# Kernel optimization log

Hardware: AMD Instinct MI355X
Metric: run time of the kernel (lower is better)

## Reference

```python
import jax, jax.numpy as jnp
import numpy as np

B, T_ENC, T_DEC = 16, 256, 200
E, ATT, PRE, H, MEL, LOC, K = 512, 128, 256, 1024, 80, 32, 31


def setup_inputs() -> dict:
    key = jax.random.key(0)
    ks = jax.random.split(key, 20)
    s = lambda k, shape: jax.random.normal(k, shape, jnp.float32) * 0.02
    return dict(
        encoder_output=jax.random.normal(ks[0], (B, T_ENC, E), jnp.float32),
        padded_mels=jax.random.normal(ks[1], (B, T_DEC, MEL), jnp.float32),
        enc_proj_w=s(ks[2], (ATT, E)),
        lstm_proj_w=s(ks[3], (ATT, H)),
        loc_conv_w=s(ks[4], (LOC, 1, K)),
        loc_conv_b=jnp.zeros((LOC,), jnp.float32),
        loc_dense_w=s(ks[5], (ATT, LOC)),
        loc_dense_b=jnp.zeros((ATT,), jnp.float32),
        e_w=s(ks[6], (1, ATT)),
        e_b=jnp.zeros((1,), jnp.float32),
        prenet1_w=s(ks[7], (PRE, MEL)),
        prenet2_w=s(ks[8], (PRE, PRE)),
        w_ih0=s(ks[9], (4 * H, PRE + E)),
        w_hh0=s(ks[10], (4 * H, H)),
        b_ih0=jnp.zeros((4 * H,), jnp.float32),
        b_hh0=jnp.zeros((4 * H,), jnp.float32),
        w_ih1=s(ks[11], (4 * H, H)),
        w_hh1=s(ks[12], (4 * H, H)),
        b_ih1=jnp.zeros((4 * H,), jnp.float32),
        b_hh1=jnp.zeros((4 * H,), jnp.float32),
        proj_w=s(ks[13], (MEL, H + E)),
        proj_b=jnp.zeros((MEL,), jnp.float32),
        stop_w=s(ks[14], (1, H + E)),
        stop_b=jnp.zeros((1,), jnp.float32),
        text_lengths=jax.random.randint(ks[15], (B,), T_ENC // 2, T_ENC + 1),
    )


def _lstm_cell_zero(x, w_ih, b_ih, b_hh):
    # PyTorch LSTM cell with zero initial (h, c): h_prev contributes nothing
    # except the recurrent bias b_hh. Gate order: i, f, g, o.
    g = x @ w_ih.T + b_ih + b_hh
    i, f, gg, o = jnp.split(g, 4, axis=-1)
    c = jax.nn.sigmoid(i) * jnp.tanh(gg)  # f * c_prev == 0
    return jax.nn.sigmoid(o) * jnp.tanh(c)


def reference(encoder_output, padded_mels, enc_proj_w, lstm_proj_w, loc_conv_w,
              loc_conv_b, loc_dense_w, loc_dense_b, e_w, e_b, prenet1_w,
              prenet2_w, w_ih0, w_hh0, b_ih0, b_hh0, w_ih1, w_hh1, b_ih1,
              b_hh1, proj_w, proj_b, stop_w, stop_b, text_lengths):
    b, t_enc, _ = encoder_output.shape
    n_mel = padded_mels.shape[-1]
    h = w_hh0.shape[-1]
    pad = (loc_conv_w.shape[-1] - 1) // 2
    proc_enc = encoder_output @ enc_proj_w.T              # [B,Te,128]
    mask = jnp.arange(t_enc)[None, :] < text_lengths[:, None]
    # teacher forcing (ratio=1.0): prev mel at step t is padded_mels[:, t-1]
    prev_mels = jnp.concatenate(
        [jnp.zeros((b, 1, n_mel), padded_mels.dtype), padded_mels[:, :-1]],
        axis=1).transpose(1, 0, 2)                        # [Td,B,80]

    def step(carry, prev_mel):
        awc, h2 = carry                                   # [B,Te], [B,1024]
        # prenet (dropout omitted for a deterministic reference)
        x = jax.nn.relu(prev_mel @ prenet1_w.T)
        x = jax.nn.relu(x @ prenet2_w.T)                  # [B,256]
        # location-sensitive attention
        q = h2 @ lstm_proj_w.T                            # [B,128]
        loc = jax.lax.conv_general_dilated(
            awc[:, None, :], loc_conv_w, (1,), [(pad, pad)],
            dimension_numbers=('NCH', 'OIH', 'NCH')) + loc_conv_b[None, :, None]
        loc = jnp.einsum('bct,ac->bta', loc, loc_dense_w) + loc_dense_b
        en = jnp.tanh(q[:, None, :] + loc + proc_enc) @ e_w[0] + e_b[0]
        en = jnp.where(mask, en, -1e9)
        aw = jax.nn.softmax(en, axis=-1)                  # [B,Te]
        ctx = jnp.einsum('bt,bte->be', aw, encoder_output)  # [B,512]
        # 2-layer LSTM, state reset to zero every step (as in the original)
        li = jnp.concatenate([x, ctx], axis=-1)           # [B,768]
        h1 = _lstm_cell_zero(li, w_ih0, b_ih0, b_hh0)
        h2n = _lstm_cell_zero(h1, w_ih1, b_ih1, b_hh1)
        dec = jnp.concatenate([h2n, ctx], axis=-1)        # [B,1536]
        mel = dec @ proj_w.T + proj_b                     # [B,80]
        stop = (dec @ stop_w.T + stop_b)[:, 0]            # [B]
        return (awc + aw, h2n), (mel, stop)

    init = (jnp.zeros((b, t_enc), encoder_output.dtype),
            jnp.zeros((b, h), encoder_output.dtype))
    _, (mels, stops) = jax.lax.scan(step, init, prev_mels)
    return mels.transpose(1, 0, 2), stops.T               # [B,Td,80], [B,Td]
```

## Files before the change

kernel.cpp:

```cpp
#include <hip/hip_runtime.h>
#include <math.h>

#define NB   16
#define TE   256
#define TD   200
#define EE   512
#define ATT  128
#define PREN 256
#define HH   1024
#define NMEL 80
#define NLOC 32
#define KWW  31
#define PADW 15

#define OFF_X2   0
#define OFF_PE   (OFF_X2 + TD*NB*PREN)
#define OFF_AWC  (OFF_PE + NB*TE*ATT)
#define OFF_EN   (OFF_AWC + NB*TE)
#define OFF_Q    (OFF_EN + NB*TE)
#define OFF_CTX  (OFF_Q + NB*ATT)
#define OFF_H1   (OFF_CTX + NB*EE)
#define OFF_H2   (OFF_H1 + NB*HH)
#define OFF_BAR  (OFF_H2 + NB*HH)
#define BAR_U32  8192

#define ARR_G  0
#define ARR_L  4096

#define LW0_F4   (12*192)
#define LW1_F4   (12*256)
#define DYN_BYTES ((LW0_F4 + LW1_F4) * 16)

typedef float f4 __attribute__((ext_vector_type(4)));

__device__ __forceinline__ float sigmf(float x) { return 1.0f / (1.0f + expf(-x)); }
__device__ __forceinline__ float dot4(f4 a, f4 b) {
  return a.x*b.x + a.y*b.y + a.z*b.z + a.w*b.w;
}
__device__ __forceinline__ float red32(float v) {
  v += __shfl_down(v, 16, 32); v += __shfl_down(v, 8, 32);
  v += __shfl_down(v, 4, 32);  v += __shfl_down(v, 2, 32);
  v += __shfl_down(v, 1, 32);
  return v;
}

__device__ __forceinline__ unsigned ld_cg_u32(const unsigned* p) {
  unsigned r;
  asm volatile("global_load_dword %0, %1, off sc0 sc1\n\ts_waitcnt vmcnt(0)"
               : "=v"(r) : "v"(p) : "memory");
  return r;
}
__device__ __forceinline__ void st_cg_u32(unsigned* p, unsigned v) {
  asm volatile("global_store_dword %0, %1, off sc0 sc1" :: "v"(p), "v"(v) : "memory");
}
__device__ __forceinline__ float ld_cg_f32(const float* p) {
  float r;
  asm volatile("global_load_dword %0, %1, off sc0 sc1\n\ts_waitcnt vmcnt(0)"
               : "=v"(r) : "v"(p) : "memory");
  return r;
}
__device__ __forceinline__ void st_cg_f32(float* p, float v) {
  asm volatile("global_store_dword %0, %1, off sc0 sc1" :: "v"(p), "v"(v) : "memory");
}
__device__ __forceinline__ f4 ld_cg_f4(const f4* p) {
  f4 r;
  asm volatile("global_load_dwordx4 %0, %1, off sc0 sc1\n\ts_waitcnt vmcnt(0)"
               : "=v"(r) : "v"(p) : "memory");
  return r;
}
__device__ __forceinline__ void st_cg_f4(f4* p, f4 v) {
  asm volatile("global_store_dwordx4 %0, %1, off sc0 sc1" :: "v"(p), "v"(v) : "memory");
}
__device__ __forceinline__ void ld4_cg(f4& r0, f4& r1, f4& r2, f4& r3,
                                       const f4* a0, const f4* a1,
                                       const f4* a2, const f4* a3) {
  asm volatile(
    "global_load_dwordx4 %0, %4, off sc0 sc1\n\t"
    "global_load_dwordx4 %1, %5, off sc0 sc1\n\t"
    "global_load_dwordx4 %2, %6, off sc0 sc1\n\t"
    "global_load_dwordx4 %3, %7, off sc0 sc1\n\t"
    "s_waitcnt vmcnt(0)"
    : "=&v"(r0), "=&v"(r1), "=&v"(r2), "=&v"(r3)
    : "v"(a0), "v"(a1), "v"(a2), "v"(a3)
    : "memory");
}
__device__ __forceinline__ void ld8_cg(f4& r0, f4& r1, f4& r2, f4& r3,
                                       f4& r4, f4& r5, f4& r6, f4& r7,
                                       const f4* a0, const f4* a1, const f4* a2,
                                       const f4* a3, const f4* a4, const f4* a5,
                                       const f4* a6, const f4* a7) {
  asm volatile(
    "global_load_dwordx4 %0, %8, off sc0 sc1\n\t"
    "global_load_dwordx4 %1, %9, off sc0 sc1\n\t"
    "global_load_dwordx4 %2, %10, off sc0 sc1\n\t"
    "global_load_dwordx4 %3, %11, off sc0 sc1\n\t"
    "global_load_dwordx4 %4, %12, off sc0 sc1\n\t"
    "global_load_dwordx4 %5, %13, off sc0 sc1\n\t"
    "global_load_dwordx4 %6, %14, off sc0 sc1\n\t"
    "global_load_dwordx4 %7, %15, off sc0 sc1\n\t"
    "s_waitcnt vmcnt(0)"
    : "=&v"(r0), "=&v"(r1), "=&v"(r2), "=&v"(r3),
      "=&v"(r4), "=&v"(r5), "=&v"(r6), "=&v"(r7)
    : "v"(a0), "v"(a1), "v"(a2), "v"(a3),
      "v"(a4), "v"(a5), "v"(a6), "v"(a7)
    : "memory");
}

__device__ __forceinline__ void g_arrive(unsigned* bar, unsigned e) {
  __syncthreads();
  if (threadIdx.x == 0) st_cg_u32(bar + ARR_G + blockIdx.x * 16, e);
}
__device__ __forceinline__ void g_wait(unsigned* bar, unsigned e) {
  if (threadIdx.x < 256) {
    while (ld_cg_u32(bar + ARR_G + threadIdx.x * 16) < e) {}
  }
  __syncthreads();
}
__device__ __forceinline__ void l_arrive(unsigned* bar, unsigned e) {
  __syncthreads();
  if (threadIdx.x == 0) st_cg_u32(bar + ARR_L + blockIdx.x * 16, e);
}
__device__ __forceinline__ void l_wait(unsigned* bar, unsigned e, int b_grp) {
  if (threadIdx.x < 16) {
    while (ld_cg_u32(bar + ARR_L + (threadIdx.x * 16 + b_grp) * 16) < e) {}
  }
  __syncthreads();
}

__global__ void k_init(float* __restrict__ ws) {
  const int tid = threadIdx.x;
  float* awc = ws + OFF_AWC;
  float* qv  = ws + OFF_Q;
  unsigned* bar = (unsigned*)(ws + OFF_BAR);
  for (int i = tid; i < NB*TE; i += 256) st_cg_f32(awc + i, 0.0f);
  for (int i = tid; i < NB*ATT; i += 256) st_cg_f32(qv + i, 0.0f);
  for (int i = tid; i < BAR_U32; i += 256) st_cg_u32(bar + i, 0u);
}

__global__ void k_prenet(const float* __restrict__ mels,
                         const float* __restrict__ w1,
                         const float* __restrict__ w2,
                         float* __restrict__ x2) {
  const int t = blockIdx.x >> 4;
  const int b = blockIdx.x & 15;
  const int j = threadIdx.x;
  __shared__ float s_in[NMEL];
  __shared__ float s_x1[PREN];
  if (j < NMEL) s_in[j] = (t == 0) ? 0.0f : mels[(b*TD + (t-1))*NMEL + j];
  __syncthreads();
  float a1 = 0.0f;
  #pragma unroll 8
  for (int k = 0; k < NMEL; ++k) a1 += s_in[k] * w1[j*NMEL + k];
  s_x1[j] = fmaxf(a1, 0.0f);
  __syncthreads();
  float a2 = 0.0f;
  #pragma unroll 8
  for (int k = 0; k < PREN; ++k) a2 += s_x1[k] * w2[j*PREN + k];
  x2[(t*NB + b)*PREN + j] = fmaxf(a2, 0.0f);
}

__global__ void k_procenc(const float* __restrict__ enc,
                          const float* __restrict__ w,
                          float* __restrict__ pe) {
  const int bt = blockIdx.x;
  const int a = threadIdx.x;
  __shared__ float s_e[EE];
  for (int k = a; k < EE; k += 128) s_e[k] = enc[bt*EE + k];
  __syncthreads();
  float acc = 0.0f;
  #pragma unroll 8
  for (int k = 0; k < EE; ++k) acc += s_e[k] * w[a*EE + k];
  pe[bt*ATT + a] = acc;
}

__global__ void __launch_bounds__(512, 1) k_main(
    const float* __restrict__ enc,
    const float* __restrict__ lstm_proj_w,
    const float* __restrict__ loc_conv_w,
    const float* __restrict__ loc_conv_b,
    const float* __restrict__ loc_dense_w,
    const float* __restrict__ loc_dense_b,
    const float* __restrict__ e_w,
    const float* __restrict__ e_b,
    const float* __restrict__ w_ih0,
    const float* __restrict__ b_ih0,
    const float* __restrict__ b_hh0,
    const float* __restrict__ w_ih1,
    const float* __restrict__ b_ih1,
    const float* __restrict__ b_hh1,
    const float* __restrict__ proj_w,
    const float* __restrict__ proj_b,
    const float* __restrict__ stop_w,
    const float* __restrict__ stop_b,
    const int*   __restrict__ text_len,
    float* __restrict__ ws,
    float* __restrict__ out) {
  const int bid = blockIdx.x;
  const int tid = threadIdx.x;

  float* x2  = ws + OFF_X2;
  float* pe  = ws + OFF_PE;
  float* awc = ws + OFF_AWC;
  float* en  = ws + OFF_EN;
  float* qv  = ws + OFF_Q;
  float* ctx = ws + OFF_CTX;
  float* h1  = ws + OFF_H1;
  float* h2  = ws + OFF_H2;
  unsigned* bar = (unsigned*)(ws + OFF_BAR);

  __shared__ __align__(16) float s_ldw[NLOC*ATT];
  __shared__ float s_awc[64];
  __shared__ float s_loc[16*33];
  __shared__ float s_red[16];
  __shared__ float s_aw[256];
  __shared__ __align__(16) float s_dec[HH+EE];
  __shared__ float s_b0[12], s_b1[12];
  extern __shared__ __align__(16) float dynlds[];
  f4* lw0 = (f4*)dynlds;
  f4* lw1 = ((f4*)dynlds) + LW0_F4;

  const int b_grp = bid & 15;
  const int sub   = bid >> 4;
  const int h0    = bid * 4;

  for (int i = tid; i < NLOC*ATT; i += 512) {
    int c = i >> 7, a = i & 127;
    s_ldw[i] = loc_dense_w[a*NLOC + c];
  }
  if (tid < 12) {
    int g = tid >> 2, h = tid & 3;
    int gr = (g == 0 ? 0 : (g == 1 ? 2048 : 3072)) + h0 + h;
    s_b0[tid] = b_ih0[gr] + b_hh0[gr];
    s_b1[tid] = b_ih1[gr] + b_hh1[gr];
  }
  {
    const f4* w0_4 = (const f4*)w_ih0;
    const f4* w1_4 = (const f4*)w_ih1;
    for (int i = tid; i < LW0_F4; i += 512) {
      int r = i / 192, c = i - r*192;
      int g = r >> 2, h = r & 3;
      int grow = (g == 0 ? 0 : (g == 1 ? 2048 : 3072)) + h0 + h;
      lw0[i] = w0_4[grow*192 + c];
    }
    for (int i = tid; i < LW1_F4; i += 512) {
      int r = i >> 8, c = i & 255;
      int g = r >> 2, h = r & 3;
      int grow = (g == 0 ? 0 : (g == 1 ? 2048 : 3072)) + h0 + h;
      lw1[i] = w1_4[grow*256 + c];
    }
  }
  const int   lenb = text_len[b_grp];
  const float eb0  = e_b[0];

  const int tl = tid >> 5;
  const int j  = tid & 31;
  float lcw_r[KWW];
  #pragma unroll
  for (int k = 0; k < KWW; ++k) lcw_r[k] = loc_conv_w[j*KWW + k];
  const float lcb_r = loc_conv_b[j];
  const f4 db_r = *(const f4*)(loc_dense_b + 4*j);
  const f4 ew_r = *(const f4*)(e_w + 4*j);
  const f4 pe_r = *(const f4*)(pe + (size_t)(b_grp*TE + sub*16 + tl)*ATT + 4*j);
  const f4 ps_r = pe_r + db_r;
  const int e4i = tid >> 6;
  const int ts  = tid & 63;
  f4 encr[4];
  {
    const f4* enc4 = (const f4*)(enc + (size_t)b_grp*TE*EE);
    #pragma unroll
    for (int i = 0; i < 4; ++i)
      encr[i] = enc4[(size_t)(ts + 64*i)*(EE/4) + sub*8 + e4i];
  }
  const int pb = tid >> 5;
  const int kc = tid & 31;
  __syncthreads();

  unsigned eg = 0, el = 0;

  for (int t = 0; t < TD; ++t) {
    f4 pre;
    {
      if (tid >= 128 && tid < 176) {
        const int i = tid - 128;
        const int g = sub*16 - PADW + i;
        s_awc[i] = (i < 46 && g >= 0 && g < TE) ? ld_cg_f32(awc + b_grp*TE + g)
                                                : 0.0f;
      }
      __syncthreads();
      float cv = lcb_r;
      #pragma unroll
      for (int k = 0; k < KWW; ++k) cv += s_awc[tl + k] * lcw_r[k];
      s_loc[tl*33 + j] = cv;
      __syncthreads();
      f4 d4 = (f4){0.f, 0.f, 0.f, 0.f};
      #pragma unroll 8
      for (int c = 0; c < NLOC; ++c) {
        const float lv = s_loc[tl*33 + c];
        const f4 w4 = ((const f4*)s_ldw)[c*32 + j];
        d4.x += lv*w4.x; d4.y += lv*w4.y; d4.z += lv*w4.z; d4.w += lv*w4.w;
      }
      pre = ps_r + d4;
    }
    l_wait(bar, el, b_grp);
    {
      const f4 q4 = ld_cg_f4((const f4*)qv + b_grp*32 + j);
      float acc = tanhf(pre.x+q4.x)*ew_r.x + tanhf(pre.y+q4.y)*ew_r.y
                + tanhf(pre.z+q4.z)*ew_r.z + tanhf(pre.w+q4.w)*ew_r.w;
      acc = red32(acc);
      if (j == 0) {
        float evv = acc + eb0;
        const int tt = sub*16 + tl;
        if (tt >= lenb) evv = -1e9f;
        st_cg_f32(en + b_grp*TE + tt, evv);
      }
    }
    l_arrive(bar, ++el);
    l_wait(bar, el, b_grp);
    {
      float evv = 0.f, p = 0.f;
      if (tid < 256) {
        evv = ld_cg_f32(en + b_grp*TE + tid);
        float m = evv;
        #pragma unroll
        for (int d = 32; d > 0; d >>= 1) m = fmaxf(m, __shfl_xor(m, d));
        if ((tid & 63) == 0) s_red[tid >> 6] = m;
      }
      __syncthreads();
      const float mx = fmaxf(fmaxf(s_red[0], s_red[1]), fmaxf(s_red[2], s_red[3]));
      if (tid < 256) {
        p = expf(evv - mx);
        float sm = p;
        #pragma unroll
        for (int d = 32; d > 0; d >>= 1) sm += __shfl_xor(sm, d);
        if ((tid & 63) == 0) s_red[8 + (tid >> 6)] = sm;
      }
      __syncthreads();
      const float inv = 1.0f / (s_red[8] + s_red[9] + s_red[10] + s_red[11]);
      if (tid < 256) {
        const float aw = p * inv;
        s_aw[tid] = aw;
        if (sub == 0) {
          const float old = ld_cg_f32(awc + b_grp*TE + tid);
          st_cg_f32(awc + b_grp*TE + tid, old + aw);
        }
      }
      __syncthreads();
      f4 a4 = (f4){0.f, 0.f, 0.f, 0.f};
      #pragma unroll
      for (int i = 0; i < 4; ++i) {
        const float awv = s_aw[ts + 64*i];
        a4.x += awv*encr[i].x; a4.y += awv*encr[i].y;
        a4.z += awv*encr[i].z; a4.w += awv*encr[i].w;
      }
      #pragma unroll
      for (int d = 32; d > 0; d >>= 1) {
        a4.x += __shfl_down(a4.x, d);
        a4.y += __shfl_down(a4.y, d);
        a4.z += __shfl_down(a4.z, d);
        a4.w += __shfl_down(a4.w, d);
      }
      if (ts == 0) st_cg_f4((f4*)ctx + b_grp*(EE/4) + sub*8 + e4i, a4);
    }
    g_arrive(bar, ++eg);
    float acc[12];
    {
      #pragma unroll
      for (int r = 0; r < 12; ++r) acc[r] = 0.0f;
      const f4* x4p = (const f4*)(x2 + (size_t)(t*NB + pb)*PREN);
      #pragma unroll
      for (int i = 0; i < 2; ++i) {
        const int kf = kc + 32*i;
        const f4 xv = x4p[kf];
        #pragma unroll
        for (int r = 0; r < 12; ++r) acc[r] += dot4(xv, lw0[r*192 + kf]);
      }
    }
    g_wait(bar, eg);
    {
      const f4* c4p = (const f4*)(ctx + pb*EE);
      f4 cv0, cv1, cv2, cv3;
      ld4_cg(cv0, cv1, cv2, cv3, c4p+kc, c4p+kc+32, c4p+kc+64, c4p+kc+96);
      #pragma unroll
      for (int r = 0; r < 12; ++r) {
        acc[r] += dot4(cv0, lw0[r*192 + 64 + kc]);
        acc[r] += dot4(cv1, lw0[r*192 + 64 + kc + 32]);
        acc[r] += dot4(cv2, lw0[r*192 + 64 + kc + 64]);
        acc[r] += dot4(cv3, lw0[r*192 + 64 + kc + 96]);
      }
      #pragma unroll
      for (int r = 0; r < 12; ++r) acc[r] = red32(acc[r]);
      if (kc == 0) {
        f4 hv;
        #pragma unroll
        for (int h = 0; h < 4; ++h) {
          const float gi = acc[h]   + s_b0[h];
          const float gg = acc[4+h] + s_b0[4+h];
          const float go = acc[8+h] + s_b0[8+h];
          const float c = sigmf(gi) * tanhf(gg);
          hv[h] = sigmf(go) * tanhf(c);
        }
        st_cg_f4((f4*)h1 + pb*(HH/4) + bid, hv);
      }
    }
    g_arrive(bar, ++eg);
    g_wait(bar, eg);
    {
      #pragma unroll
      for (int r = 0; r < 12; ++r) acc[r] = 0.0f;
      const f4* h4p = (const f4*)(h1 + pb*HH);
      f4 hv0, hv1, hv2, hv3, hv4, hv5, hv6, hv7;
      ld8_cg(hv0, hv1, hv2, hv3, hv4, hv5, hv6, hv7,
             h4p+kc, h4p+kc+32, h4p+kc+64, h4p+kc+96,
             h4p+kc+128, h4p+kc+160, h4p+kc+192, h4p+kc+224);
      #pragma unroll
      for (int r = 0; r < 12; ++r) {
        acc[r] += dot4(hv0, lw1[r*256 + kc]);
        acc[r] += dot4(hv1, lw1[r*256 + kc + 32]);
        acc[r] += dot4(hv2, lw1[r*256 + kc + 64]);
        acc[r] += dot4(hv3, lw1[r*256 + kc + 96]);
        acc[r] += dot4(hv4, lw1[r*256 + kc + 128]);
        acc[r] += dot4(hv5, lw1[r*256 + kc + 160]);
        acc[r] += dot4(hv6, lw1[r*256 + kc + 192]);
        acc[r] += dot4(hv7, lw1[r*256 + kc + 224]);
      }
      #pragma unroll
      for (int r = 0; r < 12; ++r) acc[r] = red32(acc[r]);
      if (kc == 0) {
        f4 hv;
        #pragma unroll
        for (int h = 0; h < 4; ++h) {
          const float gi = acc[h]   + s_b1[h];
          const float gg = acc[4+h] + s_b1[4+h];
          const float go = acc[8+h] + s_b1[8+h];
          const float c = sigmf(gi) * tanhf(gg);
          hv[h] = sigmf(go) * tanhf(c);
        }
        st_cg_f4((f4*)h2 + pb*(HH/4) + bid, hv);
      }
    }
    g_arrive(bar, ++eg);
    if (tid >= 256 && tid < 384)
      ((f4*)s_dec)[tid] = ld_cg_f4((const f4*)ctx + b_grp*(EE/4) + (tid - 256));
    g_wait(bar, eg);
    {
      if (tid < 256)
        ((f4*)s_dec)[tid] = ld_cg_f4((const f4*)h2 + b_grp*(HH/4) + tid);
      __syncthreads();
      const int ol = tid >> 5;
      const int kq = tid & 31;
      const f4* s4 = (const f4*)s_dec;
      if (sub < 8) {
        const int a = sub*16 + ol;
        const f4* w4 = (const f4*)(lstm_proj_w + (size_t)a*HH);
        float a2 = 0.0f;
        #pragma unroll
        for (int i = 0; i < 8; ++i) a2 += dot4(s4[kq + 32*i], w4[kq + 32*i]);
        a2 = red32(a2);
        if (kq == 0) st_cg_f32(qv + b_grp*ATT + a, a2);
      } else {
        const int m = (sub - 8)*11 + ol;
        if (ol < 11 && m < 81) {
          const float* wrow = (m < NMEL) ? (proj_w + (size_t)m*(HH+EE)) : stop_w;
          const f4* w4 = (const f4*)wrow;
          float a2 = 0.0f;
          #pragma unroll
          for (int i = 0; i < 12; ++i) a2 += dot4(s4[kq + 32*i], w4[kq + 32*i]);
          a2 = red32(a2);
          if (kq == 0) {
            if (m < NMEL) out[(b_grp*TD + t)*NMEL + m] = a2 + proj_b[m];
            else          out[NB*TD*NMEL + b_grp*TD + t] = a2 + stop_b[0];
          }
        }
      }
    }
    l_arrive(bar, ++el);
  }
}

extern "C" void kernel_launch(void* const* d_in, const int* in_sizes, int n_in,
                              void* d_out, int out_size, void* d_ws, size_t ws_size,
                              hipStream_t stream) {
  (void)in_sizes; (void)n_in; (void)out_size; (void)ws_size;
  const float* enc         = (const float*)d_in[0];
  const float* mels        = (const float*)d_in[1];
  const float* enc_proj_w  = (const float*)d_in[2];
  const float* lstm_proj_w = (const float*)d_in[3];
  const float* loc_conv_w  = (const float*)d_in[4];
  const float* loc_conv_b  = (const float*)d_in[5];
  const float* loc_dense_w = (const float*)d_in[6];
  const float* loc_dense_b = (const float*)d_in[7];
  const float* e_w         = (const float*)d_in[8];
  const float* e_b         = (const float*)d_in[9];
  const float* prenet1_w   = (const float*)d_in[10];
  const float* prenet2_w   = (const float*)d_in[11];
  const float* w_ih0       = (const float*)d_in[12];
  const float* b_ih0       = (const float*)d_in[14];
  const float* b_hh0       = (const float*)d_in[15];
  const float* w_ih1       = (const float*)d_in[16];
  const float* b_ih1       = (const float*)d_in[18];
  const float* b_hh1       = (const float*)d_in[19];
  const float* proj_w      = (const float*)d_in[20];
  const float* proj_b      = (const float*)d_in[21];
  const float* stop_w      = (const float*)d_in[22];
  const float* stop_b      = (const float*)d_in[23];
  const int*   text_len    = (const int*)d_in[24];
  float* ws  = (float*)d_ws;
  float* out = (float*)d_out;

  static int attr_set = 0;
  if (!attr_set) {
    hipFuncSetAttribute((const void*)k_main,
                        hipFuncAttributeMaxDynamicSharedMemorySize, DYN_BYTES);
    attr_set = 1;
  }

  k_init<<<dim3(1), dim3(256), 0, stream>>>(ws);
  k_prenet<<<dim3(TD*NB), dim3(256), 0, stream>>>(mels, prenet1_w, prenet2_w, ws + OFF_X2);
  k_procenc<<<dim3(NB*TE), dim3(128), 0, stream>>>(enc, enc_proj_w, ws + OFF_PE);

  k_main<<<dim3(256), dim3(512), DYN_BYTES, stream>>>(
      enc, lstm_proj_w, loc_conv_w, loc_conv_b, loc_dense_w, loc_dense_b,
      e_w, e_b, w_ih0, b_ih0, b_hh0, w_ih1, b_ih1, b_hh1,
      proj_w, proj_b, stop_w, stop_b, text_len, ws, out);
}
```

Baseline: 4.471 ms.

## Use fp16 packed activations, flag-tagged records, and defer output projection

Stores the LDS-resident LSTM weights and the exchanged activations (prenet output, context, h1, h2, query) as packed fp16 and computes the dot products with fdot2. The global barriers around h2 and q are replaced by per-record step tags that consumers poll. The attention cumulative sum now lives in each block's shared memory instead of global memory. The mel/stop projection is moved to the next step's idle window, and the query projection is split across all 16 sub-blocks. The goal is fewer grid-wide barriers and less traffic per step, at the cost of fp16 rounding error and more intricate synchronisation.

```diff
diff --git a/kernel.cpp b/kernel.cpp
--- a/kernel.cpp
+++ b/kernel.cpp
@@ -13,25 +13,27 @@
 #define KWW  31
 #define PADW 15
 
-#define OFF_X2   0
-#define OFF_PE   (OFF_X2 + TD*NB*PREN)
-#define OFF_AWC  (OFF_PE + NB*TE*ATT)
-#define OFF_EN   (OFF_AWC + NB*TE)
-#define OFF_Q    (OFF_EN + NB*TE)
-#define OFF_CTX  (OFF_Q + NB*ATT)
-#define OFF_H1   (OFF_CTX + NB*EE)
-#define OFF_H2   (OFF_H1 + NB*HH)
-#define OFF_BAR  (OFF_H2 + NB*HH)
+#define OFF_X2H  0
+#define OFF_PE   (OFF_X2H + TD*NB*128)
+#define OFF_EN   (OFF_PE + NB*TE*ATT)
+#define OFF_CTH  (OFF_EN + NB*TE)
+#define OFF_H1H  (OFF_CTH + NB*256)
+#define OFF_H2R  (OFF_H1H + NB*512)
+#define OFF_QVR  (OFF_H2R + NB*256*4)
+#define OFF_BAR  (OFF_QVR + NB*16*2*4)
 #define BAR_U32  8192
-
-#define ARR_G  0
-#define ARR_L  4096
-
-#define LW0_F4   (12*192)
-#define LW1_F4   (12*256)
-#define DYN_BYTES ((LW0_F4 + LW1_F4) * 16)
+#define ARR_G 0
+#define ARR_L 4096
+
+#define LW0X_U32 (12*128)
+#define LW0C_U32 (12*256)
+#define LW1_U32  (12*512)
+#define DYN_BYTES ((LW0X_U32 + LW0C_U32 + LW1_U32)*4)
 
 typedef float f4 __attribute__((ext_vector_type(4)));
+typedef unsigned int u32x4 __attribute__((ext_vector_type(4)));
+typedef unsigned int u32x2 __attribute__((ext_vector_type(2)));
+typedef _Float16 h2t __attribute__((ext_vector_type(2)));
 
 __device__ __forceinline__ float sigmf(float x) { return 1.0f / (1.0f + expf(-x)); }
 __device__ __forceinline__ float dot4(f4 a, f4 b) {
@@ -43,6 +45,25 @@
   v += __shfl_down(v, 1, 32);
   return v;
 }
+__device__ __forceinline__ float red64(float v) {
+  v += __shfl_down(v, 32); v += __shfl_down(v, 16); v += __shfl_down(v, 8);
+  v += __shfl_down(v, 4);  v += __shfl_down(v, 2);  v += __shfl_down(v, 1);
+  return v;
+}
+__device__ __forceinline__ float fdot2(unsigned a, unsigned b, float c) {
+  return __builtin_amdgcn_fdot2(__builtin_bit_cast(h2t, a),
+                                __builtin_bit_cast(h2t, b), c, false);
+}
+__device__ __forceinline__ unsigned pkh(float a, float b) {
+  h2t h; h.x = (_Float16)a; h.y = (_Float16)b;
+  return __builtin_bit_cast(unsigned, h);
+}
+__device__ __forceinline__ float hlo(unsigned u) {
+  return (float)__builtin_bit_cast(h2t, u).x;
+}
+__device__ __forceinline__ float hhi(unsigned u) {
+  return (float)__builtin_bit_cast(h2t, u).y;
+}
 
 __device__ __forceinline__ unsigned ld_cg_u32(const unsigned* p) {
   unsigned r;
@@ -71,39 +92,33 @@
 __device__ __forceinline__ void st_cg_f4(f4* p, f4 v) {
   asm volatile("global_store_dwordx4 %0, %1, off sc0 sc1" :: "v"(p), "v"(v) : "memory");
 }
-__device__ __forceinline__ void ld4_cg(f4& r0, f4& r1, f4& r2, f4& r3,
-                                       const f4* a0, const f4* a1,
-                                       const f4* a2, const f4* a3) {
+__device__ __forceinline__ u32x4 ld_cg_u4(const void* p) {
+  u32x4 r;
+  asm volatile("global_load_dwordx4 %0, %1, off sc0 sc1\n\ts_waitcnt vmcnt(0)"
+               : "=v"(r) : "v"(p) : "memory");
+  return r;
+}
+__device__ __forceinline__ void st_cg_u2(void* p, u32x2 v) {
+  asm volatile("global_store_dwordx2 %0, %1, off sc0 sc1" :: "v"(p), "v"(v) : "memory");
+}
+__device__ __forceinline__ void ld2u(u32x4& a, u32x4& b, const void* pa, const void* pb) {
+  asm volatile(
+    "global_load_dwordx4 %0, %2, off sc0 sc1\n\t"
+    "global_load_dwordx4 %1, %3, off sc0 sc1\n\t"
+    "s_waitcnt vmcnt(0)"
+    : "=&v"(a), "=&v"(b) : "v"(pa), "v"(pb) : "memory");
+}
+__device__ __forceinline__ void ld4u(u32x4& a, u32x4& b, u32x4& c, u32x4& d,
+                                     const void* pa, const void* pb,
+                                     const void* pc, const void* pd) {
   asm volatile(
     "global_load_dwordx4 %0, %4, off sc0 sc1\n\t"
     "global_load_dwordx4 %1, %5, off sc0 sc1\n\t"
     "global_load_dwordx4 %2, %6, off sc0 sc1\n\t"
     "global_load_dwordx4 %3, %7, off sc0 sc1\n\t"
     "s_waitcnt vmcnt(0)"
-    : "=&v"(r0), "=&v"(r1), "=&v"(r2), "=&v"(r3)
-    : "v"(a0), "v"(a1), "v"(a2), "v"(a3)
-    : "memory");
-}
-__device__ __forceinline__ void ld8_cg(f4& r0, f4& r1, f4& r2, f4& r3,
-                                       f4& r4, f4& r5, f4& r6, f4& r7,
-                                       const f4* a0, const f4* a1, const f4* a2,
-                                       const f4* a3, const f4* a4, const f4* a5,
-                                       const f4* a6, const f4* a7) {
-  asm volatile(
-    "global_load_dwordx4 %0, %8, off sc0 sc1\n\t"
-    "global_load_dwordx4 %1, %9, off sc0 sc1\n\t"
-    "global_load_dwordx4 %2, %10, off sc0 sc1\n\t"
-    "global_load_dwordx4 %3, %11, off sc0 sc1\n\t"
-    "global_load_dwordx4 %4, %12, off sc0 sc1\n\t"
-    "global_load_dwordx4 %5, %13, off sc0 sc1\n\t"
-    "global_load_dwordx4 %6, %14, off sc0 sc1\n\t"
-    "global_load_dwordx4 %7, %15, off sc0 sc1\n\t"
-    "s_waitcnt vmcnt(0)"
-    : "=&v"(r0), "=&v"(r1), "=&v"(r2), "=&v"(r3),
-      "=&v"(r4), "=&v"(r5), "=&v"(r6), "=&v"(r7)
-    : "v"(a0), "v"(a1), "v"(a2), "v"(a3),
-      "v"(a4), "v"(a5), "v"(a6), "v"(a7)
-    : "memory");
+    : "=&v"(a), "=&v"(b), "=&v"(c), "=&v"(d)
+    : "v"(pa), "v"(pb), "v"(pc), "v"(pd) : "memory");
 }
 
 __device__ __forceinline__ void g_arrive(unsigned* bar, unsigned e) {
@@ -128,19 +143,20 @@
 }
 
 __global__ void k_init(float* __restrict__ ws) {
-  const int tid = threadIdx.x;
-  float* awc = ws + OFF_AWC;
-  float* qv  = ws + OFF_Q;
+  const int gid = blockIdx.x * 256 + threadIdx.x;
+  f4* h2r = (f4*)(ws + OFF_H2R);
+  f4* qvr = (f4*)(ws + OFF_QVR);
   unsigned* bar = (unsigned*)(ws + OFF_BAR);
-  for (int i = tid; i < NB*TE; i += 256) st_cg_f32(awc + i, 0.0f);
-  for (int i = tid; i < NB*ATT; i += 256) st_cg_f32(qv + i, 0.0f);
-  for (int i = tid; i < BAR_U32; i += 256) st_cg_u32(bar + i, 0u);
+  const f4 z = (f4){0.f, 0.f, 0.f, 0.f};
+  for (int i = gid; i < NB*256; i += 32*256) st_cg_f4(h2r + i, z);
+  for (int i = gid; i < NB*16*2; i += 32*256) st_cg_f4(qvr + i, z);
+  for (int i = gid; i < BAR_U32; i += 32*256) st_cg_u32(bar + i, 0u);
 }
 
 __global__ void k_prenet(const float* __restrict__ mels,
                          const float* __restrict__ w1,
                          const float* __restrict__ w2,
-                         float* __restrict__ x2) {
+                         float* __restrict__ ws) {
   const int t = blockIdx.x >> 4;
   const int b = blockIdx.x & 15;
   const int j = threadIdx.x;
@@ -156,7 +172,7 @@
   float a2 = 0.0f;
   #pragma unroll 8
   for (int k = 0; k < PREN; ++k) a2 += s_x1[k] * w2[j*PREN + k];
-  x2[(t*NB + b)*PREN + j] = fmaxf(a2, 0.0f);
+  ((_Float16*)(ws + OFF_X2H))[((size_t)t*NB + b)*256 + j] = (_Float16)fmaxf(a2, 0.0f);
 }
 
 __global__ void k_procenc(const float* __restrict__ enc,
@@ -198,26 +214,29 @@
   const int bid = blockIdx.x;
   const int tid = threadIdx.x;
 
-  float* x2  = ws + OFF_X2;
+  const unsigned* x2h = (const unsigned*)(ws + OFF_X2H);
   float* pe  = ws + OFF_PE;
-  float* awc = ws + OFF_AWC;
   float* en  = ws + OFF_EN;
-  float* qv  = ws + OFF_Q;
-  float* ctx = ws + OFF_CTX;
-  float* h1  = ws + OFF_H1;
-  float* h2  = ws + OFF_H2;
+  unsigned* cth = (unsigned*)(ws + OFF_CTH);
+  unsigned* h1h = (unsigned*)(ws + OFF_H1H);
+  f4* h2_rec = (f4*)(ws + OFF_H2R);
+  f4* qv_rec = (f4*)(ws + OFF_QVR);
   unsigned* bar = (unsigned*)(ws + OFF_BAR);
 
   __shared__ __align__(16) float s_ldw[NLOC*ATT];
-  __shared__ float s_awc[64];
+  __shared__ float s_awcf[TE];
   __shared__ float s_loc[16*33];
   __shared__ float s_red[16];
   __shared__ float s_aw[256];
+  __shared__ float s_qtmp[8];
+  __shared__ float s_ctmp[32];
+  __shared__ __align__(16) float s_q[ATT];
   __shared__ __align__(16) float s_dec[HH+EE];
   __shared__ float s_b0[12], s_b1[12];
-  extern __shared__ __align__(16) float dynlds[];
-  f4* lw0 = (f4*)dynlds;
-  f4* lw1 = ((f4*)dynlds) + LW0_F4;
+  extern __shared__ __align__(16) unsigned dynlds_u[];
+  unsigned* lw0x = dynlds_u;
+  unsigned* lw0c = lw0x + LW0X_U32;
+  unsigned* lw1  = lw0c + LW0C_U32;
 
   const int b_grp = bid & 15;
   const int sub   = bid >> 4;
@@ -233,25 +252,31 @@
     s_b0[tid] = b_ih0[gr] + b_hh0[gr];
     s_b1[tid] = b_ih1[gr] + b_hh1[gr];
   }
-  {
-    const f4* w0_4 = (const f4*)w_ih0;
-    const f4* w1_4 = (const f4*)w_ih1;
-    for (int i = tid; i < LW0_F4; i += 512) {
-      int r = i / 192, c = i - r*192;
-      int g = r >> 2, h = r & 3;
-      int grow = (g == 0 ? 0 : (g == 1 ? 2048 : 3072)) + h0 + h;
-      lw0[i] = w0_4[grow*192 + c];
-    }
-    for (int i = tid; i < LW1_F4; i += 512) {
-      int r = i >> 8, c = i & 255;
-      int g = r >> 2, h = r & 3;
-      int grow = (g == 0 ? 0 : (g == 1 ? 2048 : 3072)) + h0 + h;
-      lw1[i] = w1_4[grow*256 + c];
-    }
-  }
+  for (int i = tid; i < LW0X_U32; i += 512) {
+    int r = i >> 7, c = i & 127;
+    int g = r >> 2, h = r & 3;
+    int grow = (g == 0 ? 0 : (g == 1 ? 2048 : 3072)) + h0 + h;
+    const float* wr = w_ih0 + (size_t)grow*768;
+    lw0x[i] = pkh(wr[2*c], wr[2*c+1]);
+  }
+  for (int i = tid; i < LW0C_U32; i += 512) {
+    int r = i >> 8, c = i & 255;
+    int g = r >> 2, h = r & 3;
+    int grow = (g == 0 ? 0 : (g == 1 ? 2048 : 3072)) + h0 + h;
+    const float* wr = w_ih0 + (size_t)grow*768 + 256;
+    lw0c[i] = pkh(wr[2*c], wr[2*c+1]);
+  }
+  for (int i = tid; i < LW1_U32; i += 512) {
+    int r = i >> 9, c = i & 511;
+    int g = r >> 2, h = r & 3;
+    int grow = (g == 0 ? 0 : (g == 1 ? 2048 : 3072)) + h0 + h;
+    const float* wr = w_ih1 + (size_t)grow*1024;
+    lw1[i] = pkh(wr[2*c], wr[2*c+1]);
+  }
+  if (tid < 256) s_awcf[tid] = 0.0f;
+
   const int   lenb = text_len[b_grp];
   const float eb0  = e_b[0];
-
   const int tl = tid >> 5;
   const int j  = tid & 31;
   float lcw_r[KWW];
@@ -278,18 +303,17 @@
   unsigned eg = 0, el = 0;
 
   for (int t = 0; t < TD; ++t) {
+    const unsigned tg = (unsigned)(t + 1);
     f4 pre;
     {
-      if (tid >= 128 && tid < 176) {
-        const int i = tid - 128;
-        const int g = sub*16 - PADW + i;
-        s_awc[i] = (i < 46 && g >= 0 && g < TE) ? ld_cg_f32(awc + b_grp*TE + g)
-                                                : 0.0f;
-      }
-      __syncthreads();
       float cv = lcb_r;
-      #pragma unroll
-      for (int k = 0; k < KWW; ++k) cv += s_awc[tl + k] * lcw_r[k];
+      const int pos = sub*16 + tl;
+      #pragma unroll
+      for (int k = 0; k < KWW; ++k) {
+        const int g = pos - PADW + k;
+        const float av = (g >= 0 && g < TE) ? s_awcf[g] : 0.0f;
+        cv += av * lcw_r[k];
+      }
       s_loc[tl*33 + j] = cv;
       __syncthreads();
       f4 d4 = (f4){0.f, 0.f, 0.f, 0.f};
@@ -301,9 +325,19 @@
       }
       pre = ps_r + d4;
     }
-    l_wait(bar, el, b_grp);
     {
-      const f4 q4 = ld_cg_f4((const f4*)qv + b_grp*32 + j);
+      if (tid < 32) {
+        const int src = tid >> 1, r = tid & 1;
+        const f4* qp = qv_rec + (b_grp*16 + src)*2 + r;
+        f4 v;
+        do { v = ld_cg_f4(qp); } while (__float_as_uint(v.z) != (unsigned)t);
+        const unsigned u0 = __float_as_uint(v.x), u1 = __float_as_uint(v.y);
+        const int base = src*8 + r*4;
+        s_q[base+0] = hlo(u0); s_q[base+1] = hhi(u0);
+        s_q[base+2] = hlo(u1); s_q[base+3] = hhi(u1);
+      }
+      __syncthreads();
+      const f4 q4 = *(const f4*)(s_q + 4*j);
       float acc = tanhf(pre.x+q4.x)*ew_r.x + tanhf(pre.y+q4.y)*ew_r.y
                 + tanhf(pre.z+q4.z)*ew_r.z + tanhf(pre.w+q4.w)*ew_r.w;
       acc = red32(acc);
@@ -315,6 +349,25 @@
       }
     }
     l_arrive(bar, ++el);
+    if (t > 0) {
+      const int ol = tid >> 5, kq = tid & 31;
+      if (ol < 6) {
+        const int m = sub*6 + ol;
+        if (m < 81) {
+          const float* wrow = (m < NMEL) ? (proj_w + (size_t)m*(HH+EE)) : stop_w;
+          const f4* w4 = (const f4*)wrow;
+          const f4* s4 = (const f4*)s_dec;
+          float a2 = 0.0f;
+          #pragma unroll
+          for (int i = 0; i < 12; ++i) a2 += dot4(s4[kq + 32*i], w4[kq + 32*i]);
+          a2 = red32(a2);
+          if (kq == 0) {
+            if (m < NMEL) out[(b_grp*TD + (t-1))*NMEL + m] = a2 + proj_b[m];
+            else          out[NB*TD*NMEL + b_grp*TD + (t-1)] = a2 + stop_b[0];
+          }
+        }
+      }
+    }
     l_wait(bar, el, b_grp);
     {
       float evv = 0.f, p = 0.f;
@@ -339,10 +392,7 @@
       if (tid < 256) {
         const float aw = p * inv;
         s_aw[tid] = aw;
-        if (sub == 0) {
-          const float old = ld_cg_f32(awc + b_grp*TE + tid);
-          st_cg_f32(awc + b_grp*TE + tid, old + aw);
-        }
+        s_awcf[tid] += aw;
       }
       __syncthreads();
       f4 a4 = (f4){0.f, 0.f, 0.f, 0.f};
@@ -352,54 +402,62 @@
         a4.x += awv*encr[i].x; a4.y += awv*encr[i].y;
         a4.z += awv*encr[i].z; a4.w += awv*encr[i].w;
       }
-      #pragma unroll
-      for (int d = 32; d > 0; d >>= 1) {
-        a4.x += __shfl_down(a4.x, d);
-        a4.y += __shfl_down(a4.y, d);
-        a4.z += __shfl_down(a4.z, d);
-        a4.w += __shfl_down(a4.w, d);
-      }
-      if (ts == 0) st_cg_f4((f4*)ctx + b_grp*(EE/4) + sub*8 + e4i, a4);
+      a4.x = red64(a4.x); a4.y = red64(a4.y); a4.z = red64(a4.z); a4.w = red64(a4.w);
+      if (ts == 0) {
+        s_ctmp[e4i*4+0] = a4.x; s_ctmp[e4i*4+1] = a4.y;
+        s_ctmp[e4i*4+2] = a4.z; s_ctmp[e4i*4+3] = a4.w;
+      }
+      __syncthreads();
+      if (tid < 4) {
+        u32x4 w;
+        w.x = pkh(s_ctmp[8*tid+0], s_ctmp[8*tid+1]);
+        w.y = pkh(s_ctmp[8*tid+2], s_ctmp[8*tid+3]);
+        w.z = pkh(s_ctmp[8*tid+4], s_ctmp[8*tid+5]);
+        w.w = pkh(s_ctmp[8*tid+6], s_ctmp[8*tid+7]);
+        u32x4* dst = (u32x4*)cth + b_grp*64 + sub*4 + tid;
+        asm volatile("global_store_dwordx4 %0, %1, off sc0 sc1" :: "v"(dst), "v"(w) : "memory");
+      }
     }
     g_arrive(bar, ++eg);
     float acc[12];
     {
       #pragma unroll
       for (int r = 0; r < 12; ++r) acc[r] = 0.0f;
-      const f4* x4p = (const f4*)(x2 + (size_t)(t*NB + pb)*PREN);
-      #pragma unroll
-      for (int i = 0; i < 2; ++i) {
-        const int kf = kc + 32*i;
-        const f4 xv = x4p[kf];
-        #pragma unroll
-        for (int r = 0; r < 12; ++r) acc[r] += dot4(xv, lw0[r*192 + kf]);
+      const u32x4 xv = ((const u32x4*)x2h)[((size_t)t*NB + pb)*32 + kc];
+      #pragma unroll
+      for (int r = 0; r < 12; ++r) {
+        const u32x4 w = ((const u32x4*)lw0x)[r*32 + kc];
+        acc[r] = fdot2(xv.x, w.x, acc[r]); acc[r] = fdot2(xv.y, w.y, acc[r]);
+        acc[r] = fdot2(xv.z, w.z, acc[r]); acc[r] = fdot2(xv.w, w.w, acc[r]);
       }
     }
     g_wait(bar, eg);
     {
-      const f4* c4p = (const f4*)(ctx + pb*EE);
-      f4 cv0, cv1, cv2, cv3;
-      ld4_cg(cv0, cv1, cv2, cv3, c4p+kc, c4p+kc+32, c4p+kc+64, c4p+kc+96);
+      u32x4 c0, c1;
+      const u32x4* cp = (const u32x4*)cth + pb*64 + kc*2;
+      ld2u(c0, c1, cp, cp + 1);
       #pragma unroll
       for (int r = 0; r < 12; ++r) {
-        acc[r] += dot4(cv0, lw0[r*192 + 64 + kc]);
-        acc[r] += dot4(cv1, lw0[r*192 + 64 + kc + 32]);
-        acc[r] += dot4(cv2, lw0[r*192 + 64 + kc + 64]);
-        acc[r] += dot4(cv3, lw0[r*192 + 64 + kc + 96]);
+        const u32x4 w0 = ((const u32x4*)lw0c)[r*64 + kc*2];
+        const u32x4 w1 = ((const u32x4*)lw0c)[r*64 + kc*2 + 1];
+        acc[r] = fdot2(c0.x, w0.x, acc[r]); acc[r] = fdot2(c0.y, w0.y, acc[r]);
+        acc[r] = fdot2(c0.z, w0.z, acc[r]); acc[r] = fdot2(c0.w, w0.w, acc[r]);
+        acc[r] = fdot2(c1.x, w1.x, acc[r]); acc[r] = fdot2(c1.y, w1.y, acc[r]);
+        acc[r] = fdot2(c1.z, w1.z, acc[r]); acc[r] = fdot2(c1.w, w1.w, acc[r]);
       }
       #pragma unroll
       for (int r = 0; r < 12; ++r) acc[r] = red32(acc[r]);
       if (kc == 0) {
-        f4 hv;
+        float hv[4];
         #pragma unroll
         for (int h = 0; h < 4; ++h) {
           const float gi = acc[h]   + s_b0[h];
           const float gg = acc[4+h] + s_b0[4+h];
           const float go = acc[8+h] + s_b0[8+h];
-          const float c = sigmf(gi) * tanhf(gg);
-          hv[h] = sigmf(go) * tanhf(c);
+          hv[h] = sigmf(go) * tanhf(sigmf(gi) * tanhf(gg));
         }
-        st_cg_f4((f4*)h1 + pb*(HH/4) + bid, hv);
+        u32x2 stv; stv.x = pkh(hv[0], hv[1]); stv.y = pkh(hv[2], hv[3]);
+        st_cg_u2((u32x2*)h1h + pb*256 + bid, stv);
       }
     }
     g_arrive(bar, ++eg);
@@ -407,73 +465,96 @@
     {
       #pragma unroll
       for (int r = 0; r < 12; ++r) acc[r] = 0.0f;
-      const f4* h4p = (const f4*)(h1 + pb*HH);
-      f4 hv0, hv1, hv2, hv3, hv4, hv5, hv6, hv7;
-      ld8_cg(hv0, hv1, hv2, hv3, hv4, hv5, hv6, hv7,
-             h4p+kc, h4p+kc+32, h4p+kc+64, h4p+kc+96,
-             h4p+kc+128, h4p+kc+160, h4p+kc+192, h4p+kc+224);
+      u32x4 v0, v1, v2, v3;
+      const u32x4* hp = (const u32x4*)h1h + pb*128 + kc*4;
+      ld4u(v0, v1, v2, v3, hp, hp+1, hp+2, hp+3);
       #pragma unroll
       for (int r = 0; r < 12; ++r) {
-        acc[r] += dot4(hv0, lw1[r*256 + kc]);
-        acc[r] += dot4(hv1, lw1[r*256 + kc + 32]);
-        acc[r] += dot4(hv2, lw1[r*256 + kc + 64]);
-        acc[r] += dot4(hv3, lw1[r*256 + kc + 96]);
-        acc[r] += dot4(hv4, lw1[r*256 + kc + 128]);
-        acc[r] += dot4(hv5, lw1[r*256 + kc + 160]);
-        acc[r] += dot4(hv6, lw1[r*256 + kc + 192]);
-        acc[r] += dot4(hv7, lw1[r*256 + kc + 224]);
+        const u32x4* wp = (const u32x4*)lw1 + r*128 + kc*4;
+        const u32x4 w0 = wp[0], w1 = wp[1], w2 = wp[2], w3 = wp[3];
+        acc[r] = fdot2(v0.x, w0.x, acc[r]); acc[r] = fdot2(v0.y, w0.y, acc[r]);
+        acc[r] = fdot2(v0.z, w0.z, acc[r]); acc[r] = fdot2(v0.w, w0.w, acc[r]);
+        acc[r] = fdot2(v1.x, w1.x, acc[r]); acc[r] = fdot2(v1.y, w1.y, acc[r]);
+        acc[r] = fdot2(v1.z, w1.z, acc[r]); acc[r] = fdot2(v1.w, w1.w, acc[r]);
+        acc[r] = fdot2(v2.x, w2.x, acc[r]); acc[r] = fdot2(v2.y, w2.y, acc[r]);
+        acc[r] = fdot2(v2.z, w2.z, acc[r]); acc[r] = fdot2(v2.w, w2.w, acc[r]);
+        acc[r] = fdot2(v3.x, w3.x, acc[r]); acc[r] = fdot2(v3.y, w3.y, acc[r]);
+        acc[r] = fdot2(v3.z, w3.z, acc[r]); acc[r] = fdot2(v3.w, w3.w, acc[r]);
       }
       #pragma unroll
       for (int r = 0; r < 12; ++r) acc[r] = red32(acc[r]);
       if (kc == 0) {
-        f4 hv;
+        float hv[4];
         #pragma unroll
         for (int h = 0; h < 4; ++h) {
           const float gi = acc[h]   + s_b1[h];
           const float gg = acc[4+h] + s_b1[4+h];
           const float go = acc[8+h] + s_b1[8+h];
-          const float c = sigmf(gi) * tanhf(gg);
-          hv[h] = sigmf(go) * tanhf(c);
+          hv[h] = sigmf(go) * tanhf(sigmf(gi) * tanhf(gg));
         }
-        st_cg_f4((f4*)h2 + pb*(HH/4) + bid, hv);
-      }
-    }
-    g_arrive(bar, ++eg);
-    if (tid >= 256 && tid < 384)
-      ((f4*)s_dec)[tid] = ld_cg_f4((const f4*)ctx + b_grp*(EE/4) + (tid - 256));
-    g_wait(bar, eg);
+        f4 r;
+        r.x = __uint_as_float(pkh(hv[0], hv[1]));
+        r.y = __uint_as_float(pkh(hv[2], hv[3]));
+        r.z = __uint_as_float(tg); r.w = 0.f;
+        st_cg_f4(h2_rec + pb*256 + bid, r);
+      }
+    }
     {
-      if (tid < 256)
-        ((f4*)s_dec)[tid] = ld_cg_f4((const f4*)h2 + b_grp*(HH/4) + tid);
-      __syncthreads();
-      const int ol = tid >> 5;
-      const int kq = tid & 31;
+      if (tid < 256) {
+        const f4* hp = h2_rec + b_grp*256 + tid;
+        f4 v;
+        do { v = ld_cg_f4(hp); } while (__float_as_uint(v.z) != tg);
+        const unsigned u0 = __float_as_uint(v.x), u1 = __float_as_uint(v.y);
+        s_dec[4*tid+0] = hlo(u0); s_dec[4*tid+1] = hhi(u0);
+        s_dec[4*tid+2] = hlo(u1); s_dec[4*tid+3] = hhi(u1);
+      } else if (tid < 320) {
+        const int i = tid - 256;
+        const u32x4 cv = ld_cg_u4((const u32x4*)cth + b_grp*64 + i);
+        s_dec[HH + 8*i + 0] = hlo(cv.x); s_dec[HH + 8*i + 1] = hhi(cv.x);
+        s_dec[HH + 8*i + 2] = hlo(cv.y); s_dec[HH + 8*i + 3] = hhi(cv.y);
+        s_dec[HH + 8*i + 4] = hlo(cv.z); s_dec[HH + 8*i + 5] = hhi(cv.z);
+        s_dec[HH + 8*i + 6] = hlo(cv.w); s_dec[HH + 8*i + 7] = hhi(cv.w);
+      }
+      __syncthreads();
+      const int row = tid >> 6;
+      const int kq  = tid & 63;
+      const int a   = sub*8 + row;
+      const f4* w4 = (const f4*)(lstm_proj_w + (size_t)a*HH);
       const f4* s4 = (const f4*)s_dec;
-      if (sub < 8) {
-        const int a = sub*16 + ol;
-        const f4* w4 = (const f4*)(lstm_proj_w + (size_t)a*HH);
+      float a2 = 0.0f;
+      #pragma unroll
+      for (int i = 0; i < 4; ++i) a2 += dot4(s4[kq + 64*i], w4[kq + 64*i]);
+      a2 = red64(a2);
+      if (kq == 0) s_qtmp[row] = a2;
+      __syncthreads();
+      if (tid < 2) {
+        f4 r;
+        r.x = __uint_as_float(pkh(s_qtmp[4*tid+0], s_qtmp[4*tid+1]));
+        r.y = __uint_as_float(pkh(s_qtmp[4*tid+2], s_qtmp[4*tid+3]));
+        r.z = __uint_as_float(tg); r.w = 0.f;
+        st_cg_f4(qv_rec + (b_grp*16 + sub)*2 + tid, r);
+      }
+    }
+  }
+  __syncthreads();
+  {
+    const int ol = tid >> 5, kq = tid & 31;
+    if (ol < 6) {
+      const int m = sub*6 + ol;
+      if (m < 81) {
+        const float* wrow = (m < NMEL) ? (proj_w + (size_t)m*(HH+EE)) : stop_w;
+        const f4* w4 = (const f4*)wrow;
+        const f4* s4 = (const f4*)s_dec;
         float a2 = 0.0f;
         #pragma unroll
-        for (int i = 0; i < 8; ++i) a2 += dot4(s4[kq + 32*i], w4[kq + 32*i]);
+        for (int i = 0; i < 12; ++i) a2 += dot4(s4[kq + 32*i], w4[kq + 32*i]);
         a2 = red32(a2);
-        if (kq == 0) st_cg_f32(qv + b_grp*ATT + a, a2);
-      } else {
-        const int m = (sub - 8)*11 + ol;
-        if (ol < 11 && m < 81) {
-          const float* wrow = (m < NMEL) ? (proj_w + (size_t)m*(HH+EE)) : stop_w;
-          const f4* w4 = (const f4*)wrow;
-          float a2 = 0.0f;
-          #pragma unroll
-          for (int i = 0; i < 12; ++i) a2 += dot4(s4[kq + 32*i], w4[kq + 32*i]);
-          a2 = red32(a2);
-          if (kq == 0) {
-            if (m < NMEL) out[(b_grp*TD + t)*NMEL + m] = a2 + proj_b[m];
-            else          out[NB*TD*NMEL + b_grp*TD + t] = a2 + stop_b[0];
-          }
+        if (kq == 0) {
+          if (m < NMEL) out[(b_grp*TD + (TD-1))*NMEL + m] = a2 + proj_b[m];
+          else          out[NB*TD*NMEL + b_grp*TD + (TD-1)] = a2 + stop_b[0];
         }
       }
     }
-    l_arrive(bar, ++el);
   }
 }
 
@@ -514,8 +595,8 @@
     attr_set = 1;
   }
 
-  k_init<<<dim3(1), dim3(256), 0, stream>>>(ws);
-  k_prenet<<<dim3(TD*NB), dim3(256), 0, stream>>>(mels, prenet1_w, prenet2_w, ws + OFF_X2);
+  k_init<<<dim3(32), dim3(256), 0, stream>>>(ws);
+  k_prenet<<<dim3(TD*NB), dim3(256), 0, stream>>>(mels, prenet1_w, prenet2_w, ws);
   k_procenc<<<dim3(NB*TE), dim3(128), 0, stream>>>(enc, enc_proj_w, ws + OFF_PE);
 
   k_main<<<dim3(256), dim3(512), DYN_BYTES, stream>>>(
```

Result: faster. 4.331 ms (-3.1%).
